# Performance work log

Measured on AMD Instinct MI355X. Metric: run time of the kernel, lower is better.

Reference implementation:

```python
import jax, jax.numpy as jnp
import numpy as np

N_NODES = 50000
N_EDGES = 800000
IN_DIM = 256
HID = 64
LAT = 64
HEADS = 4
NUM_GRAPHS = 64
NEG_SLOPE = 0.2


def _gat_layer(h_in, src, dst, W, a_s, a_d, b, heads, concat):
    N = h_in.shape[0]
    F_ = W.shape[1] // heads
    h = (h_in @ W).reshape(N, heads, F_)              # [N,H,F]
    al_s = jnp.sum(h * a_s, axis=-1)                  # [N,H]
    al_d = jnp.sum(h * a_d, axis=-1)                  # [N,H]
    e = jax.nn.leaky_relu(al_s[src] + al_d[dst], NEG_SLOPE)  # [E,H]
    # scatter-softmax over edges grouped by destination node
    m = jax.ops.segment_max(e, dst, num_segments=N)
    e = jnp.exp(e - m[dst])
    s = jax.ops.segment_sum(e, dst, num_segments=N)
    alpha = e / (s[dst] + 1e-16)                      # [E,H]
    out = jax.ops.segment_sum(h[src] * alpha[:, :, None], dst, num_segments=N)
    out = out.reshape(N, heads * F_) if concat else out.mean(axis=1)
    return out + b


def setup_inputs() -> dict:
    key = jax.random.key(0)
    ks = jax.random.split(key, 20)
    g = lambda k, shp, sc: jax.random.normal(k, shp, jnp.float32) * sc
    inp = {}
    inp['x'] = g(ks[0], (N_NODES, IN_DIM), 1.0)
    inp['edge_index'] = jax.random.randint(ks[1], (2, N_EDGES), 0, N_NODES, jnp.int32)
    inp['batch'] = jnp.sort(jax.random.randint(ks[2], (N_NODES,), 0, NUM_GRAPHS, jnp.int32))
    # layer 0: IN_DIM -> HID, 4 heads, concat
    inp['W1'] = g(ks[3], (IN_DIM, HEADS * HID), 0.05)
    inp['a1s'] = g(ks[4], (HEADS, HID), 0.05)
    inp['a1d'] = g(ks[5], (HEADS, HID), 0.05)
    inp['b1'] = jnp.zeros((HEADS * HID,), jnp.float32)
    # layer 1: 4*HID -> HID, 4 heads, concat
    inp['W2'] = g(ks[6], (HEADS * HID, HEADS * HID), 0.05)
    inp['a2s'] = g(ks[7], (HEADS, HID), 0.05)
    inp['a2d'] = g(ks[8], (HEADS, HID), 0.05)
    inp['b2'] = jnp.zeros((HEADS * HID,), jnp.float32)
    # layer 2: 4*HID -> LAT, 1 head, mean
    inp['W3'] = g(ks[9], (HEADS * HID, LAT), 0.05)
    inp['a3s'] = g(ks[10], (1, LAT), 0.05)
    inp['a3d'] = g(ks[11], (1, LAT), 0.05)
    inp['b3'] = jnp.zeros((LAT,), jnp.float32)
    # VAE head
    inp['Wmu'] = g(ks[12], (LAT, LAT), 0.1)
    inp['bmu'] = jnp.zeros((LAT,), jnp.float32)
    inp['Wlv'] = g(ks[13], (LAT, LAT), 0.1)
    inp['blv'] = jnp.zeros((LAT,), jnp.float32)
    return inp


def reference(x, edge_index, batch, W1, a1s, a1d, b1, W2, a2s, a2d, b2,
              W3, a3s, a3d, b3, Wmu, bmu, Wlv, blv):
    N = x.shape[0]
    loop = jnp.arange(N, dtype=edge_index.dtype)
    src = jnp.concatenate([edge_index[0], loop])   # add self-loops (PyG default)
    dst = jnp.concatenate([edge_index[1], loop])
    h = _gat_layer(x, src, dst, W1, a1s, a1d, b1, HEADS, True)
    h = jax.nn.elu(h)
    h = _gat_layer(h, src, dst, W2, a2s, a2d, b2, HEADS, True)
    h = jax.nn.elu(h)
    h = _gat_layer(h, src, dst, W3, a3s, a3d, b3, 1, False)
    # global mean pool per graph
    sums = jax.ops.segment_sum(h, batch, num_segments=NUM_GRAPHS)
    cnts = jax.ops.segment_sum(jnp.ones((N,), h.dtype), batch, num_segments=NUM_GRAPHS)
    pooled = sums / jnp.maximum(cnts, 1.0)[:, None]  # [G, LAT]
    mu = pooled @ Wmu + bmu
    logvar = pooled @ Wlv + blv
    std = jnp.exp(0.5 * logvar)
    eps = jax.random.normal(jax.random.key(42), std.shape, std.dtype)
    z = mu + eps * std
    return (mu, logvar, z)
```

## Files before the change

kernel.cpp:

```cpp
#include <hip/hip_runtime.h>
#include <hip/hip_bf16.h>
#include <cstdint>
#include <math.h>


#define N_NODES 50000
#define N_EDGES 800000
#define NEG_SLOPE 0.2f
#define CAP 128

typedef __hip_bfloat16 bf16;
typedef short short8 __attribute__((ext_vector_type(8)));
typedef float floatx4 __attribute__((ext_vector_type(4)));
typedef float floatx2 __attribute__((ext_vector_type(2)));

__device__ __forceinline__ float bf2f(bf16 v){ return __bfloat162float(v); }
__device__ __forceinline__ float bflo(unsigned u){ union{unsigned u; float f;} c; c.u = u<<16; return c.f; }
__device__ __forceinline__ float bfhi(unsigned u){ union{unsigned u; float f;} c; c.u = u & 0xFFFF0000u; return c.f; }
__device__ __forceinline__ float leaky(float v){ return v>0.f ? v : NEG_SLOPE*v; }
__device__ __forceinline__ unsigned short f2bu(float f){
  union{ bf16 b; unsigned short u; } c; c.b = __float2bfloat16(f); return c.u;
}
__device__ __forceinline__ unsigned char f2fp8(float v){
  int p = __builtin_amdgcn_cvt_pk_fp8_f32(v, v, 0, false);
  return (unsigned char)(p & 0xff);
}
__device__ __forceinline__ void acc_fp8x4(float* acc, unsigned wrd, float wgt){
  floatx2 lo = __builtin_amdgcn_cvt_pk_f32_fp8((int)wrd, false);
  floatx2 hi = __builtin_amdgcn_cvt_pk_f32_fp8((int)wrd, true);
  acc[0] = fmaf(lo[0], wgt, acc[0]);
  acc[1] = fmaf(lo[1], wgt, acc[1]);
  acc[2] = fmaf(hi[0], wgt, acc[2]);
  acc[3] = fmaf(hi[1], wgt, acc[3]);
}

__device__ __forceinline__ void tf_round(unsigned& x0, unsigned& x1, int r){
  x0 += x1; x1 = (x1<<r)|(x1>>(32-r)); x1 ^= x0;
}
__device__ __forceinline__ void threefry2x32(unsigned k0, unsigned k1, unsigned& x0, unsigned& x1){
  unsigned ks2 = k0 ^ k1 ^ 0x1BD11BDAu;
  x0 += k0; x1 += k1;
  tf_round(x0,x1,13); tf_round(x0,x1,15); tf_round(x0,x1,26); tf_round(x0,x1,6);
  x0 += k1; x1 += ks2 + 1u;
  tf_round(x0,x1,17); tf_round(x0,x1,29); tf_round(x0,x1,16); tf_round(x0,x1,24);
  x0 += ks2; x1 += k0 + 2u;
  tf_round(x0,x1,13); tf_round(x0,x1,15); tf_round(x0,x1,26); tf_round(x0,x1,6);
  x0 += k0; x1 += k1 + 3u;
  tf_round(x0,x1,17); tf_round(x0,x1,29); tf_round(x0,x1,16); tf_round(x0,x1,24);
  x0 += k1; x1 += ks2 + 4u;
  tf_round(x0,x1,13); tf_round(x0,x1,15); tf_round(x0,x1,26); tf_round(x0,x1,6);
  x0 += ks2; x1 += k0 + 5u;
}

__device__ __forceinline__ float erfinv_approx(float x){
  float w = -log1pf(-x*x);
  float p;
  if (w < 5.0f){
    w = w - 2.5f;
    p = 2.81022636e-08f;
    p = fmaf(p,w,3.43273939e-07f);
    p = fmaf(p,w,-3.5233877e-06f);
    p = fmaf(p,w,-4.39150654e-06f);
    p = fmaf(p,w,0.00021858087f);
    p = fmaf(p,w,-0.00125372503f);
    p = fmaf(p,w,-0.00417768164f);
    p = fmaf(p,w,0.246640727f);
    p = fmaf(p,w,1.50140941f);
  } else {
    w = sqrtf(w) - 3.0f;
    p = -0.000200214257f;
    p = fmaf(p,w,0.000100950558f);
    p = fmaf(p,w,0.00134934322f);
    p = fmaf(p,w,-0.00367342844f);
    p = fmaf(p,w,0.00573950773f);
    p = fmaf(p,w,-0.0076224613f);
    p = fmaf(p,w,0.00943887047f);
    p = fmaf(p,w,1.00167406f);
    p = fmaf(p,w,2.83297682f);
  }
  return p*x;
}

__global__ __launch_bounds__(256) void wt_all_kernel(
        const float* __restrict__ W1, const float* __restrict__ W2,
        const float* __restrict__ W3, short* __restrict__ Wt1,
        short* __restrict__ Wt2, short* __restrict__ Wt3){
  const float* W; short* Wt; int Nn;
  if (blockIdx.z == 0){ W = W1; Wt = Wt1; Nn = 256; }
  else if (blockIdx.z == 1){ W = W2; Wt = Wt2; Nn = 256; }
  else { W = W3; Wt = Wt3; Nn = 64; }
  const int n0 = blockIdx.x*32, k0 = blockIdx.y*32;
  if (n0 >= Nn) return;
  __shared__ float tile[32][33];
  const int tx = threadIdx.x & 31, ty = threadIdx.x >> 5;
  #pragma unroll
  for (int i=0;i<4;++i)
    tile[ty+8*i][tx] = W[(size_t)(k0+ty+8*i)*Nn + n0 + tx];
  __syncthreads();
  #pragma unroll
  for (int i=0;i<4;++i)
    Wt[(size_t)(n0+ty+8*i)*256 + k0 + tx] = (short)f2bu(tile[tx][ty+8*i]);
}

template<int OUT, bool INBF>
__global__ __launch_bounds__(256) void gemm_mfma_kernel(const void* __restrict__ inp,
        const short* __restrict__ Wt, void* __restrict__ outv,
        const float* __restrict__ a_s, const float* __restrict__ a_d,
        float* __restrict__ als, float* __restrict__ ald, int N){
  constexpr int M_BLK = (OUT==256) ? 64 : 256;
  constexpr int H = (OUT==256) ? 4 : 1;
  __shared__ short As[M_BLK*48];
  __shared__ short Bs[OUT*48];
  const int t = threadIdx.x;
  const int w = t>>6, lane = t&63;
  const int lm = lane&15, g = lane>>4;
  const int m0 = blockIdx.x * M_BLK;
  const int m_off = (OUT==256) ? 0 : w*64;
  const int n0    = (OUT==256) ? w*64 : 0;

  floatx4 acc[4][4] = {};

  for (int kk=0; kk<8; ++kk){
    const int k0 = kk*32;
    __syncthreads();
    for (int a = t; a < M_BLK*4; a += 256){
      int r = a>>2, c = a&3;
      int gr = m0 + r;
      uint4 v = make_uint4(0u,0u,0u,0u);
      if (gr < N){
        if constexpr (INBF){
          v = *(const uint4*)((const bf16*)inp + (size_t)gr*256 + k0 + c*8);
        } else {
          const float* p = (const float*)inp + (size_t)gr*256 + k0 + c*8;
          float4 f0 = *(const float4*)p;
          float4 f1 = *(const float4*)(p+4);
          v.x = (unsigned)f2bu(f0.x) | ((unsigned)f2bu(f0.y)<<16);
          v.y = (unsigned)f2bu(f0.z) | ((unsigned)f2bu(f0.w)<<16);
          v.z = (unsigned)f2bu(f1.x) | ((unsigned)f2bu(f1.y)<<16);
          v.w = (unsigned)f2bu(f1.z) | ((unsigned)f2bu(f1.w)<<16);
        }
      }
      *(uint4*)&As[r*48 + c*8] = v;
    }
    for (int a = t; a < OUT*4; a += 256){
      int r = a>>2, c = a&3;
      uint4 v = *(const uint4*)(Wt + (size_t)r*256 + k0 + c*8);
      *(uint4*)&Bs[r*48 + c*8] = v;
    }
    __syncthreads();
    short8 af[4], bfr[4];
    #pragma unroll
    for (int mt=0;mt<4;++mt)
      af[mt] = *(const short8*)&As[(m_off + mt*16 + lm)*48 + g*8];
    #pragma unroll
    for (int nt=0;nt<4;++nt)
      bfr[nt] = *(const short8*)&Bs[(n0 + nt*16 + lm)*48 + g*8];
    #pragma unroll
    for (int mt=0;mt<4;++mt)
      #pragma unroll
      for (int nt=0;nt<4;++nt)
        acc[mt][nt] = __builtin_amdgcn_mfma_f32_16x16x32_bf16(af[mt], bfr[nt], acc[mt][nt], 0, 0, 0);
  }

  float asv[4], adv[4];
  #pragma unroll
  for (int nt=0;nt<4;++nt){
    asv[nt] = a_s[n0 + nt*16 + lm];
    adv[nt] = a_d[n0 + nt*16 + lm];
  }
  const int head = (OUT==256) ? w : 0;
  #pragma unroll
  for (int mt=0;mt<4;++mt){
    #pragma unroll
    for (int reg=0;reg<4;++reg){
      int gr = m0 + m_off + mt*16 + g*4 + reg;
      bool valid = gr < N;
      float ps = 0.f, pd = 0.f;
      #pragma unroll
      for (int nt=0;nt<4;++nt){
        float v = acc[mt][nt][reg];
        if (valid){
          if constexpr (OUT==256){
            ((unsigned char*)outv)[(size_t)gr*256 + n0 + nt*16 + lm] = f2fp8(v);
          } else {
            ((bf16*)outv)[(size_t)gr*OUT + n0 + nt*16 + lm] = __float2bfloat16(v);
          }
        }
        ps = fmaf(v, asv[nt], ps);
        pd = fmaf(v, adv[nt], pd);
      }
      #pragma unroll
      for (int o=1;o<16;o<<=1){ ps += __shfl_xor(ps,o); pd += __shfl_xor(pd,o); }
      if (lm==0 && valid){
        als[gr*H + head] = ps;
        ald[gr*H + head] = pd;
      }
    }
  }
}

__global__ void build_kernel(const int* __restrict__ ei, int* __restrict__ deg,
        unsigned short* __restrict__ csr, int E, int N){
  int e = blockIdx.x*blockDim.x+threadIdx.x;
  if (e >= E+N) return;
  int s_ = (e < E) ? ei[e]   : e-E;
  int d_ = (e < E) ? ei[E+e] : e-E;
  int r = atomicAdd(&deg[d_], 1);
  if (r < CAP) csr[(size_t)d_*CAP + r] = (unsigned short)s_;
}

template<bool ELU>
__global__ __launch_bounds__(64) void aggregate4_kernel(const unsigned char* __restrict__ h8,
        const float* __restrict__ als, const float* __restrict__ ald,
        const int* __restrict__ deg, const unsigned short* __restrict__ csr,
        const float* __restrict__ bias, bf16* __restrict__ out){
  __shared__ int   s_src[64];
  __shared__ float s_w[64][4];
  const int n = blockIdx.x, lane = threadIdx.x;
  const int r = lane>>4;
  const int f = lane&15;
  const int head = f>>2;
  const int p0 = n*CAP;
  const int cnt = min(deg[n], CAP);
  const float4 aldn4 = *(const float4*)(ald + n*4);
  float ssum = 0.f;
  float acc[16] = {};
  for (int c=0; c<cnt; c+=64){
    int e = c + lane;
    int src = n; float4 w4 = make_float4(0.f,0.f,0.f,0.f);
    if (e < cnt){
      src = (int)csr[p0+e];
      float4 av = *(const float4*)(als + src*4);
      w4.x = expf(leaky(av.x + aldn4.x));
      w4.y = expf(leaky(av.y + aldn4.y));
      w4.z = expf(leaky(av.z + aldn4.z));
      w4.w = expf(leaky(av.w + aldn4.w));
    }
    s_src[lane] = src;
    *(float4*)&s_w[lane][0] = w4;
    int ce = min(64, cnt - c);
    int cp = (ce+7)&~7;
    for (int i=0;i<cp;i+=8){
      int src0 = s_src[i+r], src1 = s_src[i+4+r];
      float w0 = s_w[i+r][head], w1 = s_w[i+4+r][head];
      uint4 h0 = *(const uint4*)(h8 + (size_t)src0*256 + f*16);
      uint4 h1 = *(const uint4*)(h8 + (size_t)src1*256 + f*16);
      ssum += w0 + w1;
      acc_fp8x4(acc+0,  h0.x, w0); acc_fp8x4(acc+4,  h0.y, w0);
      acc_fp8x4(acc+8,  h0.z, w0); acc_fp8x4(acc+12, h0.w, w0);
      acc_fp8x4(acc+0,  h1.x, w1); acc_fp8x4(acc+4,  h1.y, w1);
      acc_fp8x4(acc+8,  h1.z, w1); acc_fp8x4(acc+12, h1.w, w1);
    }
  }
  #pragma unroll
  for (int j=0;j<16;++j){
    acc[j] += __shfl_xor(acc[j], 16);
    acc[j] += __shfl_xor(acc[j], 32);
  }
  ssum += __shfl_xor(ssum, 16);
  ssum += __shfl_xor(ssum, 32);
  if (r==0){
    float inv = 1.f/(ssum + 1e-16f);
    #pragma unroll
    for (int half=0; half<2; ++half){
      float4 b0 = *(const float4*)(bias + f*16 + half*8);
      float4 b1 = *(const float4*)(bias + f*16 + half*8 + 4);
      float rv[8];
      rv[0]=acc[half*8+0]*inv+b0.x; rv[1]=acc[half*8+1]*inv+b0.y;
      rv[2]=acc[half*8+2]*inv+b0.z; rv[3]=acc[half*8+3]*inv+b0.w;
      rv[4]=acc[half*8+4]*inv+b1.x; rv[5]=acc[half*8+5]*inv+b1.y;
      rv[6]=acc[half*8+6]*inv+b1.z; rv[7]=acc[half*8+7]*inv+b1.w;
      union{ bf16 b[8]; uint4 u; } pk;
      #pragma unroll
      for (int j=0;j<8;++j){
        float v = rv[j];
        if (ELU) v = (v>0.f)?v:expm1f(v);
        pk.b[j] = __float2bfloat16(v);
      }
      *(uint4*)(out + (size_t)n*256 + f*16 + half*8) = pk.u;
    }
  }
}

__global__ __launch_bounds__(64) void aggregate1_kernel(const bf16* __restrict__ h,
        const float* __restrict__ als, const float* __restrict__ ald,
        const int* __restrict__ deg, const unsigned short* __restrict__ csr,
        const float* __restrict__ bias, bf16* __restrict__ out){
  __shared__ int   s_src[64];
  __shared__ float s_w[64];
  const int n = blockIdx.x, lane = threadIdx.x;
  const int r = lane>>4;
  const int f = lane&15;
  const int p0 = n*CAP;
  const int cnt = min(deg[n], CAP);
  const float aldn = ald[n];
  float ssum = 0.f;
  float acc[4] = {};
  for (int c=0; c<cnt; c+=64){
    int e = c + lane;
    int src = n; float wv = 0.f;
    if (e < cnt){
      src = (int)csr[p0+e];
      wv = expf(leaky(als[src] + aldn));
    }
    s_src[lane] = src; s_w[lane] = wv;
    int ce = min(64, cnt - c);
    int cp = (ce+7)&~7;
    for (int i=0;i<cp;i+=8){
      int src0 = s_src[i+r], src1 = s_src[i+4+r];
      float w0 = s_w[i+r],   w1 = s_w[i+4+r];
      uint2 h0 = *(const uint2*)(h + (size_t)src0*64 + f*4);
      uint2 h1 = *(const uint2*)(h + (size_t)src1*64 + f*4);
      ssum += w0 + w1;
      acc[0]=fmaf(bflo(h0.x),w0,acc[0]); acc[1]=fmaf(bfhi(h0.x),w0,acc[1]);
      acc[2]=fmaf(bflo(h0.y),w0,acc[2]); acc[3]=fmaf(bfhi(h0.y),w0,acc[3]);
      acc[0]=fmaf(bflo(h1.x),w1,acc[0]); acc[1]=fmaf(bfhi(h1.x),w1,acc[1]);
      acc[2]=fmaf(bflo(h1.y),w1,acc[2]); acc[3]=fmaf(bfhi(h1.y),w1,acc[3]);
    }
  }
  #pragma unroll
  for (int j=0;j<4;++j){
    acc[j] += __shfl_xor(acc[j], 16);
    acc[j] += __shfl_xor(acc[j], 32);
  }
  ssum += __shfl_xor(ssum, 16);
  ssum += __shfl_xor(ssum, 32);
  if (r==0){
    float inv = 1.f/(ssum + 1e-16f);
    union{ bf16 b[4]; uint2 u; } pk;
    #pragma unroll
    for (int j=0;j<4;++j) pk.b[j] = __float2bfloat16(acc[j]*inv + bias[f*4+j]);
    *(uint2*)(out + (size_t)n*64 + f*4) = pk.u;
  }
}

__global__ __launch_bounds__(64) void pool_kernel(const bf16* __restrict__ h3,
        const int* __restrict__ batch, float* __restrict__ psum, float* __restrict__ pcnt,
        int N, int chunk){
  int n0 = blockIdx.x*chunk;
  if (n0 >= N) return;
  int n1 = min(N, n0+chunk);
  int t = threadIdx.x;
  int gcur = batch[n0];
  float acc = 0.f, cnt = 0.f;
  for (int n=n0; n<n1; ++n){
    int g = batch[n];
    if (g != gcur){
      atomicAdd(&psum[gcur*64+t], acc);
      if (t==0) atomicAdd(&pcnt[gcur], cnt);
      acc = 0.f; cnt = 0.f; gcur = g;
    }
    acc += bf2f(h3[(size_t)n*64+t]);
    cnt += 1.f;
  }
  atomicAdd(&psum[gcur*64+t], acc);
  if (t==0) atomicAdd(&pcnt[gcur], cnt);
}

__global__ __launch_bounds__(64) void head_kernel(const float* __restrict__ psum,
        const float* __restrict__ pcnt,
        const float* __restrict__ Wmu, const float* __restrict__ bmu,
        const float* __restrict__ Wlv, const float* __restrict__ blv,
        float* __restrict__ out){
  int g = blockIdx.x, t = threadIdx.x;
  __shared__ float p[64];
  float cnt = fmaxf(pcnt[g], 1.0f);
  p[t] = psum[g*64+t] / cnt;
  __syncthreads();
  float mu = bmu[t], lv = blv[t];
  for (int k=0;k<64;++k){
    float pk = p[k];
    mu = fmaf(pk, Wmu[(size_t)k*64+t], mu);
    lv = fmaf(pk, Wlv[(size_t)k*64+t], lv);
  }
  int i = g*64 + t;
  unsigned x0 = 0u, x1 = (unsigned)i;
  threefry2x32(0u, 42u, x0, x1);
  unsigned bits = x0 ^ x1;
  float f = __uint_as_float((bits>>9) | 0x3F800000u) - 1.0f;
  const float lo = __uint_as_float(0xBF7FFFFFu);
  float u = fmaxf(lo, f*2.0f + lo);
  float eps = 1.41421356f * erfinv_approx(u);
  float z = mu + eps * expf(0.5f*lv);
  out[i]        = mu;
  out[4096 + i] = lv;
  out[8192 + i] = z;
}

extern "C" void kernel_launch(void* const* d_in, const int* in_sizes, int n_in,
                              void* d_out, int out_size, void* d_ws, size_t ws_size,
                              hipStream_t stream){
  const float* x    = (const float*)d_in[0];
  const int*   ei   = (const int*)d_in[1];
  const int*   batch= (const int*)d_in[2];
  const float* W1   = (const float*)d_in[3];
  const float* a1s  = (const float*)d_in[4];
  const float* a1d  = (const float*)d_in[5];
  const float* b1   = (const float*)d_in[6];
  const float* W2   = (const float*)d_in[7];
  const float* a2s  = (const float*)d_in[8];
  const float* a2d  = (const float*)d_in[9];
  const float* b2   = (const float*)d_in[10];
  const float* W3   = (const float*)d_in[11];
  const float* a3s  = (const float*)d_in[12];
  const float* a3d  = (const float*)d_in[13];
  const float* b3   = (const float*)d_in[14];
  const float* Wmu  = (const float*)d_in[15];
  const float* bmu  = (const float*)d_in[16];
  const float* Wlv  = (const float*)d_in[17];
  const float* blv  = (const float*)d_in[18];
  float* out = (float*)d_out;

  const int N = N_NODES, E = N_EDGES;
  const int ET = E + N;

  char* ws = (char*)d_ws;
  size_t o = 0;
  auto alloc = [&](size_t bytes)->void*{
    void* p = ws + o; o += (bytes + 255) & ~(size_t)255; return p;
  };
  bf16*  hA      = (bf16*) alloc((size_t)N*256*2);
  unsigned char* hB8 = (unsigned char*)alloc((size_t)N*256);
  bf16*  h3      = (bf16*) alloc((size_t)N*64*2);
  float* als     = (float*)alloc((size_t)N*4*4);
  float* ald     = (float*)alloc((size_t)N*4*4);
  int*   deg     = (int*)  alloc((size_t)N*4);
  unsigned short* csr16 = (unsigned short*)alloc((size_t)N*CAP*2);
  short* Wt1     = (short*)alloc(256*256*2);
  short* Wt2     = (short*)alloc(256*256*2);
  short* Wt3     = (short*)alloc(64*256*2);
  float* psum    = (float*)alloc(64*64*4 + 64*4);
  float* pcnt    = psum + 64*64;
  (void)ws_size; (void)n_in; (void)in_sizes; (void)out_size;

  const int TB = 256;

  wt_all_kernel<<<dim3(8,8,3), 256, 0, stream>>>(W1, W2, W3, Wt1, Wt2, Wt3);

  hipMemsetAsync(deg, 0, (size_t)N*4, stream);
  build_kernel<<<(ET+TB-1)/TB, TB, 0, stream>>>(ei, deg, csr16, E, N);

  gemm_mfma_kernel<256,false><<<(N+63)/64, 256, 0, stream>>>(x, Wt1, hB8, a1s, a1d, als, ald, N);
  aggregate4_kernel<true><<<N, 64, 0, stream>>>(hB8, als, ald, deg, csr16, b1, hA);

  gemm_mfma_kernel<256,true><<<(N+63)/64, 256, 0, stream>>>(hA, Wt2, hB8, a2s, a2d, als, ald, N);
  aggregate4_kernel<true><<<N, 64, 0, stream>>>(hB8, als, ald, deg, csr16, b2, hA);

  gemm_mfma_kernel<64,true><<<(N+255)/256, 256, 0, stream>>>(hA, Wt3, h3, a3s, a3d, als, ald, N);
  aggregate1_kernel<<<N, 64, 0, stream>>>(h3, als, ald, deg, csr16, b3, hA);

  hipMemsetAsync(psum, 0, 64*64*4 + 64*4, stream);
  const int PBLK = 512;
  const int chunk = (N + PBLK - 1)/PBLK;
  pool_kernel<<<PBLK, 64, 0, stream>>>(hA, batch, psum, pcnt, N, chunk);
  head_kernel<<<64, 64, 0, stream>>>(psum, pcnt, Wmu, bmu, Wlv, blv, out);
}
```

Baseline: 418.2 us.

## Split GAT aggregation across heads/feature slices into separate blocks per node

The aggregation kernels now launch one 64-thread block per (node, head) for the 4-head layers and per (node, feature half) for the final layer, instead of one block per node. Each block covers a narrower 64-byte slice of the source row, so more edges are processed in parallel per iteration, and the partial sums are reduced with extra shuffles. The aim is more blocks and memory-level parallelism for these latency-bound gathers. The cost is that CSR indices and attention weights are reloaded and recomputed per slice, and each gather becomes narrower and less coalesced.

```diff
diff --git a/kernel.cpp b/kernel.cpp
--- a/kernel.cpp
+++ b/kernel.cpp
@@ -215,36 +215,33 @@
         const int* __restrict__ deg, const unsigned short* __restrict__ csr,
         const float* __restrict__ bias, bf16* __restrict__ out){
   __shared__ int   s_src[64];
-  __shared__ float s_w[64][4];
-  const int n = blockIdx.x, lane = threadIdx.x;
-  const int r = lane>>4;
-  const int f = lane&15;
-  const int head = f>>2;
+  __shared__ float s_w[64];
+  const int b = blockIdx.x;
+  const int n = b >> 2, s = b & 3;
+  const int lane = threadIdx.x;
+  const int r = lane>>2;
+  const int f = lane&3;
   const int p0 = n*CAP;
   const int cnt = min(deg[n], CAP);
-  const float4 aldn4 = *(const float4*)(ald + n*4);
+  const float aldn = ald[n*4 + s];
   float ssum = 0.f;
   float acc[16] = {};
   for (int c=0; c<cnt; c+=64){
     int e = c + lane;
-    int src = n; float4 w4 = make_float4(0.f,0.f,0.f,0.f);
+    int src = n; float wv = 0.f;
     if (e < cnt){
       src = (int)csr[p0+e];
-      float4 av = *(const float4*)(als + src*4);
-      w4.x = expf(leaky(av.x + aldn4.x));
-      w4.y = expf(leaky(av.y + aldn4.y));
-      w4.z = expf(leaky(av.z + aldn4.z));
-      w4.w = expf(leaky(av.w + aldn4.w));
+      wv = expf(leaky(als[src*4 + s] + aldn));
     }
     s_src[lane] = src;
-    *(float4*)&s_w[lane][0] = w4;
+    s_w[lane] = wv;
     int ce = min(64, cnt - c);
-    int cp = (ce+7)&~7;
-    for (int i=0;i<cp;i+=8){
-      int src0 = s_src[i+r], src1 = s_src[i+4+r];
-      float w0 = s_w[i+r][head], w1 = s_w[i+4+r][head];
-      uint4 h0 = *(const uint4*)(h8 + (size_t)src0*256 + f*16);
-      uint4 h1 = *(const uint4*)(h8 + (size_t)src1*256 + f*16);
+    int cp = (ce+31)&~31;
+    for (int i=0;i<cp;i+=32){
+      int src0 = s_src[i+r], src1 = s_src[i+16+r];
+      float w0 = s_w[i+r],   w1 = s_w[i+16+r];
+      uint4 h0 = *(const uint4*)(h8 + (size_t)src0*256 + s*64 + f*16);
+      uint4 h1 = *(const uint4*)(h8 + (size_t)src1*256 + s*64 + f*16);
       ssum += w0 + w1;
       acc_fp8x4(acc+0,  h0.x, w0); acc_fp8x4(acc+4,  h0.y, w0);
       acc_fp8x4(acc+8,  h0.z, w0); acc_fp8x4(acc+12, h0.w, w0);
@@ -254,17 +251,22 @@
   }
   #pragma unroll
   for (int j=0;j<16;++j){
+    acc[j] += __shfl_xor(acc[j], 4);
+    acc[j] += __shfl_xor(acc[j], 8);
     acc[j] += __shfl_xor(acc[j], 16);
     acc[j] += __shfl_xor(acc[j], 32);
   }
+  ssum += __shfl_xor(ssum, 4);
+  ssum += __shfl_xor(ssum, 8);
   ssum += __shfl_xor(ssum, 16);
   ssum += __shfl_xor(ssum, 32);
   if (r==0){
     float inv = 1.f/(ssum + 1e-16f);
+    const float* bp = bias + s*64 + f*16;
     #pragma unroll
     for (int half=0; half<2; ++half){
-      float4 b0 = *(const float4*)(bias + f*16 + half*8);
-      float4 b1 = *(const float4*)(bias + f*16 + half*8 + 4);
+      float4 b0 = *(const float4*)(bp + half*8);
+      float4 b1 = *(const float4*)(bp + half*8 + 4);
       float rv[8];
       rv[0]=acc[half*8+0]*inv+b0.x; rv[1]=acc[half*8+1]*inv+b0.y;
       rv[2]=acc[half*8+2]*inv+b0.z; rv[3]=acc[half*8+3]*inv+b0.w;
@@ -277,7 +279,7 @@
         if (ELU) v = (v>0.f)?v:expm1f(v);
         pk.b[j] = __float2bfloat16(v);
       }
-      *(uint4*)(out + (size_t)n*256 + f*16 + half*8) = pk.u;
+      *(uint4*)(out + (size_t)n*256 + s*64 + f*16 + half*8) = pk.u;
     }
   }
 }
@@ -288,9 +290,11 @@
         const float* __restrict__ bias, bf16* __restrict__ out){
   __shared__ int   s_src[64];
   __shared__ float s_w[64];
-  const int n = blockIdx.x, lane = threadIdx.x;
-  const int r = lane>>4;
-  const int f = lane&15;
+  const int b = blockIdx.x;
+  const int n = b >> 1, s = b & 1;
+  const int lane = threadIdx.x;
+  const int r = lane>>3;
+  const int f = lane&7;
   const int p0 = n*CAP;
   const int cnt = min(deg[n], CAP);
   const float aldn = ald[n];
@@ -305,12 +309,12 @@
     }
     s_src[lane] = src; s_w[lane] = wv;
     int ce = min(64, cnt - c);
-    int cp = (ce+7)&~7;
-    for (int i=0;i<cp;i+=8){
-      int src0 = s_src[i+r], src1 = s_src[i+4+r];
-      float w0 = s_w[i+r],   w1 = s_w[i+4+r];
-      uint2 h0 = *(const uint2*)(h + (size_t)src0*64 + f*4);
-      uint2 h1 = *(const uint2*)(h + (size_t)src1*64 + f*4);
+    int cp = (ce+15)&~15;
+    for (int i=0;i<cp;i+=16){
+      int src0 = s_src[i+r], src1 = s_src[i+8+r];
+      float w0 = s_w[i+r],   w1 = s_w[i+8+r];
+      uint2 h0 = *(const uint2*)(h + (size_t)src0*64 + s*32 + f*4);
+      uint2 h1 = *(const uint2*)(h + (size_t)src1*64 + s*32 + f*4);
       ssum += w0 + w1;
       acc[0]=fmaf(bflo(h0.x),w0,acc[0]); acc[1]=fmaf(bfhi(h0.x),w0,acc[1]);
       acc[2]=fmaf(bflo(h0.y),w0,acc[2]); acc[3]=fmaf(bfhi(h0.y),w0,acc[3]);
@@ -320,17 +324,19 @@
   }
   #pragma unroll
   for (int j=0;j<4;++j){
+    acc[j] += __shfl_xor(acc[j], 8);
     acc[j] += __shfl_xor(acc[j], 16);
     acc[j] += __shfl_xor(acc[j], 32);
   }
+  ssum += __shfl_xor(ssum, 8);
   ssum += __shfl_xor(ssum, 16);
   ssum += __shfl_xor(ssum, 32);
   if (r==0){
     float inv = 1.f/(ssum + 1e-16f);
     union{ bf16 b[4]; uint2 u; } pk;
     #pragma unroll
-    for (int j=0;j<4;++j) pk.b[j] = __float2bfloat16(acc[j]*inv + bias[f*4+j]);
-    *(uint2*)(out + (size_t)n*64 + f*4) = pk.u;
+    for (int j=0;j<4;++j) pk.b[j] = __float2bfloat16(acc[j]*inv + bias[s*32 + f*4 + j]);
+    *(uint2*)(out + (size_t)n*64 + s*32 + f*4) = pk.u;
   }
 }
 
@@ -441,13 +447,13 @@
   build_kernel<<<(ET+TB-1)/TB, TB, 0, stream>>>(ei, deg, csr16, E, N);
 
   gemm_mfma_kernel<256,false><<<(N+63)/64, 256, 0, stream>>>(x, Wt1, hB8, a1s, a1d, als, ald, N);
-  aggregate4_kernel<true><<<N, 64, 0, stream>>>(hB8, als, ald, deg, csr16, b1, hA);
+  aggregate4_kernel<true><<<4*N, 64, 0, stream>>>(hB8, als, ald, deg, csr16, b1, hA);
 
   gemm_mfma_kernel<256,true><<<(N+63)/64, 256, 0, stream>>>(hA, Wt2, hB8, a2s, a2d, als, ald, N);
-  aggregate4_kernel<true><<<N, 64, 0, stream>>>(hB8, als, ald, deg, csr16, b2, hA);
+  aggregate4_kernel<true><<<4*N, 64, 0, stream>>>(hB8, als, ald, deg, csr16, b2, hA);
 
   gemm_mfma_kernel<64,true><<<(N+255)/256, 256, 0, stream>>>(hA, Wt3, h3, a3s, a3d, als, ald, N);
-  aggregate1_kernel<<<N, 64, 0, stream>>>(h3, als, ald, deg, csr16, b3, hA);
+  aggregate1_kernel<<<2*N, 64, 0, stream>>>(h3, als, ald, deg, csr16, b3, hA);
 
   hipMemsetAsync(psum, 0, 64*64*4 + 64*4, stream);
   const int PBLK = 512;
```

Result: slower. 627.1 us (+50.0%).

## Fuse layer-1 GEMM with CSR build and pack four nodes per aggregate block

Applied to the files above, without the earlier changes.

The layer-1 GEMM and the edge-bucket build become one launch, with the first blocks doing the GEMM and the remaining blocks doing the atomic CSR fill, so the two independent jobs overlap and one launch is dropped. The aggregate kernels now run four 64-thread wavefronts per 256-thread block, one node per wavefront, with per-wave shared buffers. This cuts the block count and scheduling overhead for the aggregates. Every block in the fused kernel reserves the GEMM's shared memory, including the build blocks that never use it, which can limit how many build blocks are resident at once.

```diff
diff --git a/kernel.cpp b/kernel.cpp
--- a/kernel.cpp
+++ b/kernel.cpp
@@ -8,6 +8,7 @@
 #define N_EDGES 800000
 #define NEG_SLOPE 0.2f
 #define CAP 128
+#define GB1 ((N_NODES+63)/64)
 
 typedef __hip_bfloat16 bf16;
 typedef short short8 __attribute__((ext_vector_type(8)));
@@ -103,18 +104,17 @@
 }
 
 template<int OUT, bool INBF>
-__global__ __launch_bounds__(256) void gemm_mfma_kernel(const void* __restrict__ inp,
+__device__ __forceinline__ void gemm_body(int bx, const void* __restrict__ inp,
         const short* __restrict__ Wt, void* __restrict__ outv,
         const float* __restrict__ a_s, const float* __restrict__ a_d,
-        float* __restrict__ als, float* __restrict__ ald, int N){
+        float* __restrict__ als, float* __restrict__ ald, int N,
+        short* As, short* Bs){
   constexpr int M_BLK = (OUT==256) ? 64 : 256;
   constexpr int H = (OUT==256) ? 4 : 1;
-  __shared__ short As[M_BLK*48];
-  __shared__ short Bs[OUT*48];
   const int t = threadIdx.x;
   const int w = t>>6, lane = t&63;
   const int lm = lane&15, g = lane>>4;
-  const int m0 = blockIdx.x * M_BLK;
+  const int m0 = bx * M_BLK;
   const int m_off = (OUT==256) ? 0 : w*64;
   const int n0    = (OUT==256) ? w*64 : 0;
 
@@ -199,24 +199,51 @@
   }
 }
 
-__global__ void build_kernel(const int* __restrict__ ei, int* __restrict__ deg,
-        unsigned short* __restrict__ csr, int E, int N){
-  int e = blockIdx.x*blockDim.x+threadIdx.x;
-  if (e >= E+N) return;
-  int s_ = (e < E) ? ei[e]   : e-E;
-  int d_ = (e < E) ? ei[E+e] : e-E;
-  int r = atomicAdd(&deg[d_], 1);
-  if (r < CAP) csr[(size_t)d_*CAP + r] = (unsigned short)s_;
+template<int OUT, bool INBF>
+__global__ __launch_bounds__(256) void gemm_mfma_kernel(const void* __restrict__ inp,
+        const short* __restrict__ Wt, void* __restrict__ outv,
+        const float* __restrict__ a_s, const float* __restrict__ a_d,
+        float* __restrict__ als, float* __restrict__ ald, int N){
+  constexpr int M_BLK = (OUT==256) ? 64 : 256;
+  __shared__ short As[M_BLK*48];
+  __shared__ short Bs[OUT*48];
+  gemm_body<OUT,INBF>((int)blockIdx.x, inp, Wt, outv, a_s, a_d, als, ald, N, As, Bs);
+}
+
+__global__ __launch_bounds__(256) void fused_g1_build_kernel(
+        const float* __restrict__ x, const short* __restrict__ Wt1,
+        unsigned char* __restrict__ hB8,
+        const float* __restrict__ a1s, const float* __restrict__ a1d,
+        float* __restrict__ als, float* __restrict__ ald,
+        const int* __restrict__ ei, int* __restrict__ deg,
+        unsigned short* __restrict__ csr){
+  __shared__ short As[64*48];
+  __shared__ short Bs[256*48];
+  const int bx = (int)blockIdx.x;
+  if (bx < GB1){
+    gemm_body<256,false>(bx, x, Wt1, hB8, a1s, a1d, als, ald, N_NODES, As, Bs);
+  } else {
+    int idx = (bx - GB1)*256 + (int)threadIdx.x;
+    if (idx < N_EDGES + N_NODES){
+      int s_ = (idx < N_EDGES) ? ei[idx]          : idx - N_EDGES;
+      int d_ = (idx < N_EDGES) ? ei[N_EDGES+idx]  : idx - N_EDGES;
+      int r = atomicAdd(&deg[d_], 1);
+      if (r < CAP) csr[(size_t)d_*CAP + r] = (unsigned short)s_;
+    }
+  }
 }
 
 template<bool ELU>
-__global__ __launch_bounds__(64) void aggregate4_kernel(const unsigned char* __restrict__ h8,
+__global__ __launch_bounds__(256) void aggregate4_kernel(const unsigned char* __restrict__ h8,
         const float* __restrict__ als, const float* __restrict__ ald,
         const int* __restrict__ deg, const unsigned short* __restrict__ csr,
         const float* __restrict__ bias, bf16* __restrict__ out){
-  __shared__ int   s_src[64];
-  __shared__ float s_w[64][4];
-  const int n = blockIdx.x, lane = threadIdx.x;
+  __shared__ int   s_src[4][64];
+  __shared__ float s_w[4][64][4];
+  const int wv_ = threadIdx.x >> 6;
+  const int n = blockIdx.x*4 + wv_;
+  if (n >= N_NODES) return;
+  const int lane = threadIdx.x & 63;
   const int r = lane>>4;
   const int f = lane&15;
   const int head = f>>2;
@@ -236,13 +263,13 @@
       w4.z = expf(leaky(av.z + aldn4.z));
       w4.w = expf(leaky(av.w + aldn4.w));
     }
-    s_src[lane] = src;
-    *(float4*)&s_w[lane][0] = w4;
+    s_src[wv_][lane] = src;
+    *(float4*)&s_w[wv_][lane][0] = w4;
     int ce = min(64, cnt - c);
     int cp = (ce+7)&~7;
     for (int i=0;i<cp;i+=8){
-      int src0 = s_src[i+r], src1 = s_src[i+4+r];
-      float w0 = s_w[i+r][head], w1 = s_w[i+4+r][head];
+      int src0 = s_src[wv_][i+r], src1 = s_src[wv_][i+4+r];
+      float w0 = s_w[wv_][i+r][head], w1 = s_w[wv_][i+4+r][head];
       uint4 h0 = *(const uint4*)(h8 + (size_t)src0*256 + f*16);
       uint4 h1 = *(const uint4*)(h8 + (size_t)src1*256 + f*16);
       ssum += w0 + w1;
@@ -282,13 +309,16 @@
   }
 }
 
-__global__ __launch_bounds__(64) void aggregate1_kernel(const bf16* __restrict__ h,
+__global__ __launch_bounds__(256) void aggregate1_kernel(const bf16* __restrict__ h,
         const float* __restrict__ als, const float* __restrict__ ald,
         const int* __restrict__ deg, const unsigned short* __restrict__ csr,
         const float* __restrict__ bias, bf16* __restrict__ out){
-  __shared__ int   s_src[64];
-  __shared__ float s_w[64];
-  const int n = blockIdx.x, lane = threadIdx.x;
+  __shared__ int   s_src[4][64];
+  __shared__ float s_w[4][64];
+  const int wv_ = threadIdx.x >> 6;
+  const int n = blockIdx.x*4 + wv_;
+  if (n >= N_NODES) return;
+  const int lane = threadIdx.x & 63;
   const int r = lane>>4;
   const int f = lane&15;
   const int p0 = n*CAP;
@@ -303,12 +333,12 @@
       src = (int)csr[p0+e];
       wv = expf(leaky(als[src] + aldn));
     }
-    s_src[lane] = src; s_w[lane] = wv;
+    s_src[wv_][lane] = src; s_w[wv_][lane] = wv;
     int ce = min(64, cnt - c);
     int cp = (ce+7)&~7;
     for (int i=0;i<cp;i+=8){
-      int src0 = s_src[i+r], src1 = s_src[i+4+r];
-      float w0 = s_w[i+r],   w1 = s_w[i+4+r];
+      int src0 = s_src[wv_][i+r], src1 = s_src[wv_][i+4+r];
+      float w0 = s_w[wv_][i+r],   w1 = s_w[wv_][i+4+r];
       uint2 h0 = *(const uint2*)(h + (size_t)src0*64 + f*4);
       uint2 h1 = *(const uint2*)(h + (size_t)src1*64 + f*4);
       ssum += w0 + w1;
@@ -433,21 +463,20 @@
   float* pcnt    = psum + 64*64;
   (void)ws_size; (void)n_in; (void)in_sizes; (void)out_size;
 
-  const int TB = 256;
-
   wt_all_kernel<<<dim3(8,8,3), 256, 0, stream>>>(W1, W2, W3, Wt1, Wt2, Wt3);
 
   hipMemsetAsync(deg, 0, (size_t)N*4, stream);
-  build_kernel<<<(ET+TB-1)/TB, TB, 0, stream>>>(ei, deg, csr16, E, N);
-
-  gemm_mfma_kernel<256,false><<<(N+63)/64, 256, 0, stream>>>(x, Wt1, hB8, a1s, a1d, als, ald, N);
-  aggregate4_kernel<true><<<N, 64, 0, stream>>>(hB8, als, ald, deg, csr16, b1, hA);
+
+  const int buildBlocks = (ET + 255)/256;
+  fused_g1_build_kernel<<<GB1 + buildBlocks, 256, 0, stream>>>(
+      x, Wt1, hB8, a1s, a1d, als, ald, ei, deg, csr16);
+  aggregate4_kernel<true><<<(N+3)/4, 256, 0, stream>>>(hB8, als, ald, deg, csr16, b1, hA);
 
   gemm_mfma_kernel<256,true><<<(N+63)/64, 256, 0, stream>>>(hA, Wt2, hB8, a2s, a2d, als, ald, N);
-  aggregate4_kernel<true><<<N, 64, 0, stream>>>(hB8, als, ald, deg, csr16, b2, hA);
+  aggregate4_kernel<true><<<(N+3)/4, 256, 0, stream>>>(hB8, als, ald, deg, csr16, b2, hA);
 
   gemm_mfma_kernel<64,true><<<(N+255)/256, 256, 0, stream>>>(hA, Wt3, h3, a3s, a3d, als, ald, N);
-  aggregate1_kernel<<<N, 64, 0, stream>>>(h3, als, ald, deg, csr16, b3, hA);
+  aggregate1_kernel<<<(N+3)/4, 256, 0, stream>>>(h3, als, ald, deg, csr16, b3, hA);
 
   hipMemsetAsync(psum, 0, 64*64*4 + 64*4, stream);
   const int PBLK = 512;
```

New measurement: 433.1 us. 3.6% more time.
